# Kernel tuning notes

Measured on AMD Instinct MI355X. Metric: run time of the kernel, lower is better.

Reference implementation:

```python
import jax, jax.numpy as jnp
import numpy as np

# Decode-stage paged attention with ALiBi (HPU flat-PA style):
# batch2block scatter of queries, per-block QK + alibi bias, segment-wise
# stable softmax over each sequence's blocks, AV matmul, block2batch reduce.
BATCH = 32          # decode sequences
H = 32              # query heads
KVH = 8             # kv heads (GQA)
QPK = H // KVH      # queries per kv head
D = 128             # head size
BS = 128            # block size (tokens per KV-cache block)
BLOCKS_PER_SEQ = 16 # context 2048 tokens per sequence
U = BATCH * BLOCKS_PER_SEQ  # 512 used blocks
NB = 600            # total blocks in cache pool
SCALE = 1.0 / float(np.sqrt(D))
NEG = -1e30


def setup_inputs() -> dict:
    key = jax.random.key(0)
    k0, k1, k2 = jax.random.split(key, 3)
    query = jax.random.normal(k0, (BATCH, H, D), jnp.float32)
    key_cache = jax.random.normal(k1, (NB, BS, KVH, D), jnp.float32)
    value_cache = jax.random.normal(k2, (NB, BS, KVH, D), jnp.float32)
    # contiguous PA: used blocks are the first U blocks of the pool
    block_list = jnp.arange(U, dtype=jnp.int32)
    # each sequence owns BLOCKS_PER_SEQ consecutive blocks
    block_groups = (jnp.arange(U, dtype=jnp.int32) // BLOCKS_PER_SEQ).astype(jnp.int32)
    # all blocks fully used (context = BLOCKS_PER_SEQ*BS exactly)
    block_usage = jnp.full((U,), BS, dtype=jnp.int32)
    # alibi_blocks[u, p] = (global position) - (context_len - 1)  (<= 0)
    ctx = BLOCKS_PER_SEQ * BS
    pos = (jnp.arange(U) % BLOCKS_PER_SEQ)[:, None] * BS + jnp.arange(BS)[None, :]
    alibi_blocks = (pos - (ctx - 1)).astype(jnp.float32)
    # standard geometric alibi slopes: 2^(-8*(i+1)/H)
    alibi_slopes = 2.0 ** (-(jnp.arange(1, H + 1, dtype=jnp.float32)) * (8.0 / H))
    return dict(query=query, key_cache=key_cache, value_cache=value_cache,
                alibi_blocks=alibi_blocks, alibi_slopes=alibi_slopes,
                block_list=block_list, block_groups=block_groups,
                block_usage=block_usage)


def reference(query, key_cache, value_cache, alibi_blocks, alibi_slopes,
              block_list, block_groups, block_usage):
    # gather KV blocks from the paged cache
    K = key_cache[block_list]            # [U, BS, KVH, D]
    V = value_cache[block_list]          # [U, BS, KVH, D]
    # batch2block: replicate each sequence's query onto its blocks
    q = query[block_groups] * SCALE      # [U, H, D]
    qg = q.reshape(U, KVH, QPK, D)
    # QK^T per block (GQA: each kv head serves QPK query heads)
    scores = jnp.einsum('ugqd,ukgd->ugqk', qg, K).reshape(U, H, BS)
    # decode alibi bias: [U, H, BS] = alibi_blocks[:,None,:] * slopes[None,:,None]
    scores = scores + alibi_blocks[:, None, :] * alibi_slopes[None, :, None]
    # mask unused slots within each block
    valid = jnp.arange(BS, dtype=jnp.int32)[None, :] < block_usage[:, None]  # [U, BS]
    scores = jnp.where(valid[:, None, :], scores, NEG)
    # stable softmax across all blocks of each sequence (segment-wise)
    bmax = scores.max(-1)                                            # [U, H]
    gmax = jax.ops.segment_max(bmax, block_groups, num_segments=BATCH)
    e = jnp.exp(scores - gmax[block_groups][:, :, None])             # [U, H, BS]
    e = jnp.where(valid[:, None, :], e, 0.0)
    bsum = e.sum(-1)                                                 # [U, H]
    gsum = jax.ops.segment_sum(bsum, block_groups, num_segments=BATCH)  # [B, H]
    # AV per block, then block2batch reduce
    eg = e.reshape(U, KVH, QPK, BS)
    av = jnp.einsum('ugqk,ukgd->ugqd', eg, V).reshape(U, H, D)       # [U, H, D]
    out = jax.ops.segment_sum(av, block_groups, num_segments=BATCH)  # [B, H, D]
    out = out / gsum[:, :, None]
    return out.reshape(BATCH, H * D)
```

## Files before the change

kernel.cpp:

```cpp
#include <hip/hip_runtime.h>
#include <stdint.h>

#define BATCH 32
#define NH    32
#define KVH   8
#define QPK   4
#define DH    128
#define BS    128
#define NEG   (-1e30f)
#define SCALEF 0.08838834764831845f
#define MAXU  64
#define NSP   8
#define CHK   8
#define KVROW (KVH * DH)

#define GAS __attribute__((address_space(1)))
#define LAS __attribute__((address_space(3)))

#define LOAD_V(PB, VR) do {                                                     \
  const float* vb_ = value_cache + ((size_t)(PB) * BS + T0 + half) * KVROW      \
                   + g * DH + r32 * 4;                                          \
  _Pragma("unroll")                                                             \
  for (int tp = 0; tp < 4; ++tp)                                                \
    VR[tp] = *(const float4*)&vb_[(size_t)tp * 2 * KVROW];                      \
} while (0)

#define STAGE_K(PB, BUFI) do {                                                  \
  const float* kbase_ = key_cache + ((size_t)(PB) * BS + T0) * KVROW + g * DH;  \
  float* dst_ = &Kbuf[w][BUFI][0];                                              \
  _Pragma("unroll")                                                             \
  for (int seg = 0; seg < 4; ++seg) {                                           \
    const int t_  = 2 * seg + half;                                             \
    const int sg_ = r32 ^ t_;                                                   \
    __builtin_amdgcn_global_load_lds(                                           \
        (const GAS void*)(kbase_ + (size_t)t_ * KVROW + sg_ * 4),               \
        (LAS void*)(dst_ + seg * 256), 16, 0, 0);                               \
  }                                                                             \
} while (0)

#define COMPUTE(BUFI, ABV) do {                                                 \
  const float* kb_ = &Kbuf[w][BUFI][0];                                         \
  float a0_ = 0.f, a1_ = 0.f, a2_ = 0.f, a3_ = 0.f;                             \
  _Pragma("unroll")                                                             \
  for (int i = 0; i < 4; ++i) {                                                 \
    const int gi_  = oc * 4 + i;                                                \
    const int pos_ = gi_ ^ r8;                                                  \
    const float4 kv = *(const float4*)&kb_[r8 * DH + pos_ * 4];                 \
    const float4 q0 = *(const float4*)&q_lds[0 * DH + gi_ * 4];                 \
    const float4 q1 = *(const float4*)&q_lds[1 * DH + gi_ * 4];                 \
    const float4 q2 = *(const float4*)&q_lds[2 * DH + gi_ * 4];                 \
    const float4 q3 = *(const float4*)&q_lds[3 * DH + gi_ * 4];                 \
    a0_ += kv.x*q0.x + kv.y*q0.y + kv.z*q0.z + kv.w*q0.w;                       \
    a1_ += kv.x*q1.x + kv.y*q1.y + kv.z*q1.z + kv.w*q1.w;                       \
    a2_ += kv.x*q2.x + kv.y*q2.y + kv.z*q2.z + kv.w*q2.w;                       \
    a3_ += kv.x*q3.x + kv.y*q3.y + kv.z*q3.z + kv.w*q3.w;                       \
  }                                                                             \
  float accv_[QPK] = {a0_, a1_, a2_, a3_};                                      \
  const bool valid_ = (T0 + r8) < us_c;                                         \
  float pr_[QPK];                                                               \
  _Pragma("unroll")                                                             \
  for (int qh = 0; qh < QPK; ++qh) {                                            \
    float sc = accv_[qh];                                                       \
    sc += __shfl_xor(sc, 8);  sc += __shfl_xor(sc, 16); sc += __shfl_xor(sc, 32);\
    sc += (ABV) * slope[qh];                                                    \
    if (!valid_) sc = NEG;                                                      \
    float cm = fmaxf(sc, __shfl_xor(sc, 1));                                    \
    cm = fmaxf(cm, __shfl_xor(cm, 2)); cm = fmaxf(cm, __shfl_xor(cm, 4));       \
    const float mnew = fmaxf(m[qh], cm);                                        \
    const float rs = __expf(m[qh] - mnew);                                      \
    m[qh] = mnew;                                                               \
    pr_[qh] = valid_ ? __expf(sc - mnew) : 0.f;                                 \
    sacc[qh] = sacc[qh] * rs + ((lane < 8) ? pr_[qh] : 0.f);                    \
    O[qh][0] *= rs; O[qh][1] *= rs; O[qh][2] *= rs; O[qh][3] *= rs;             \
  }                                                                             \
  if (lane < 8)                                                                 \
    *(float4*)&p_lds[w][r8 * 4] = make_float4(pr_[0], pr_[1], pr_[2], pr_[3]);  \
} while (0)

#define AV(VR) do {                                                             \
  _Pragma("unroll")                                                             \
  for (int tp = 0; tp < 4; ++tp) {                                              \
    const float4 pv = *(const float4*)&p_lds[w][(2 * tp + half) * 4];           \
    const float4 vv = VR[tp];                                                   \
    O[0][0]+=pv.x*vv.x; O[0][1]+=pv.x*vv.y; O[0][2]+=pv.x*vv.z; O[0][3]+=pv.x*vv.w; \
    O[1][0]+=pv.y*vv.x; O[1][1]+=pv.y*vv.y; O[1][2]+=pv.y*vv.z; O[1][3]+=pv.y*vv.w; \
    O[2][0]+=pv.z*vv.x; O[2][1]+=pv.z*vv.y; O[2][2]+=pv.z*vv.z; O[2][3]+=pv.z*vv.w; \
    O[3][0]+=pv.w*vv.x; O[3][1]+=pv.w*vv.y; O[3][2]+=pv.w*vv.z; O[3][3]+=pv.w*vv.w; \
  }                                                                             \
} while (0)

#define BODY(VCUR, VNXT, BUFC, BUFN, CIDX) do {                                 \
  __builtin_amdgcn_sched_barrier(0);                                            \
  asm volatile("s_waitcnt vmcnt(0)" ::: "memory");                              \
  __builtin_amdgcn_sched_barrier(0);                                            \
  const bool hn_ = (CIDX) + 1 < nblk;                                           \
  int u_n = 0, pb_n = 0, us_n = 0; float ab_n = 0.f;                            \
  if (hn_) {                                                                    \
    u_n = ulist[(CIDX) + 1]; pb_n = pblds[(CIDX) + 1]; us_n = uslds[(CIDX) + 1];\
    LOAD_V(pb_n, VNXT);                                                         \
    ab_n = alibi_blocks[(size_t)u_n * BS + T0 + r8];                            \
    __builtin_amdgcn_sched_barrier(0);                                          \
    STAGE_K(pb_n, BUFN);                                                        \
    __builtin_amdgcn_sched_barrier(0);                                          \
  }                                                                             \
  COMPUTE(BUFC, ab_c);                                                          \
  AV(VCUR);                                                                     \
  u_c = u_n; pb_c = pb_n; us_c = us_n; ab_c = ab_n;                             \
} while (0)

__global__ __launch_bounds__(128, 4)
void pa_partial(const float* __restrict__ query,
                const float* __restrict__ key_cache,
                const float* __restrict__ value_cache,
                const float* __restrict__ alibi_blocks,
                const float* __restrict__ alibi_slopes,
                const int* __restrict__ block_list,
                const int* __restrict__ block_groups,
                const int* __restrict__ block_usage,
                float* __restrict__ Mp, float* __restrict__ Sp,
                float* __restrict__ Op, int U) {
  __shared__ __align__(16) float Kbuf[2][2][CHK * DH];
  __shared__ __align__(16) float q_lds[QPK * DH];
  __shared__ __align__(16) float p_lds[2][CHK * QPK];
  __shared__ int ulist[MAXU], pblds[MAXU], uslds[MAXU];
  __shared__ int ucount;

  const int tid  = threadIdx.x;
  const int w    = tid >> 6;
  const int lane = tid & 63;
  const int r32  = lane & 31;
  const int half = lane >> 5;
  const int r8   = lane & 7;
  const int oc   = lane >> 3;
  const int bid  = blockIdx.x;
  const int b    = bid >> 6;
  const int g    = (bid >> 3) & 7;
  const int s    = bid & 7;
  const int T0   = s * 16 + w * CHK;

  if (w == 0) {
    int cnt = 0;
    for (int base = 0; base < U; base += 64) {
      const int u = base + lane;
      const bool match = (u < U) && (block_groups[u] == b);
      const unsigned long long mk = __ballot(match);
      if (match) {
        const int pre = __popcll(mk & ((1ull << lane) - 1ull));
        if (cnt + pre < MAXU) ulist[cnt + pre] = u;
      }
      cnt += __popcll(mk);
    }
    if (cnt > MAXU) cnt = MAXU;
    if (lane == 0) ucount = cnt;
    for (int i = lane; i < cnt; i += 64) {
      const int u = ulist[i];
      pblds[i] = block_list[u];
      uslds[i] = block_usage[u];
    }
  }

  {
    const float* qsrc = query + ((size_t)b * NH + g * QPK) * DH;
    for (int e = tid; e < QPK * DH; e += 128) q_lds[e] = qsrc[e] * SCALEF;
  }

  float slope[QPK];
#pragma unroll
  for (int qh = 0; qh < QPK; ++qh) slope[qh] = alibi_slopes[g * QPK + qh];

  __syncthreads();

  const int nblk = ucount;

  float m[QPK], sacc[QPK], O[QPK][4];
#pragma unroll
  for (int qh = 0; qh < QPK; ++qh) {
    m[qh] = NEG; sacc[qh] = 0.f;
#pragma unroll
    for (int k = 0; k < 4; ++k) O[qh][k] = 0.f;
  }

  float4 vA[4], vB[4];
  int u_c = 0, pb_c = 0, us_c = 0;
  float ab_c = 0.f;

  if (nblk > 0) {
    u_c = ulist[0]; pb_c = pblds[0]; us_c = uslds[0];
    LOAD_V(pb_c, vA);
    ab_c = alibi_blocks[(size_t)u_c * BS + T0 + r8];
    STAGE_K(pb_c, 0);
  }

  for (int c = 0; c < nblk; c += 2) {
    BODY(vA, vB, 0, 1, c);
    if (c + 1 < nblk) BODY(vB, vA, 1, 0, c + 1);
  }

  float* cO  = &Kbuf[w][0][0];
  float* cMS = &Kbuf[w][1][0];
#pragma unroll
  for (int qh = 0; qh < QPK; ++qh) {
    float sv = sacc[qh];
#pragma unroll
    for (int off = 1; off < 64; off <<= 1) sv += __shfl_xor(sv, off);
#pragma unroll
    for (int k = 0; k < 4; ++k) O[qh][k] += __shfl_xor(O[qh][k], 32);
    if (half == 0) {
#pragma unroll
      for (int k = 0; k < 4; ++k) cO[qh * DH + r32 * 4 + k] = O[qh][k];
    }
    if (lane == 0) { cMS[qh] = m[qh]; cMS[4 + qh] = sv; }
  }
  __syncthreads();

  for (int e = tid; e < QPK * DH; e += 128) {
    const int qh = e >> 7, d = e & 127;
    const float M  = fmaxf(Kbuf[0][1][qh], Kbuf[1][1][qh]);
    const float f0 = __expf(Kbuf[0][1][qh] - M);
    const float f1 = __expf(Kbuf[1][1][qh] - M);
    const float S  = f0 * Kbuf[0][1][4 + qh] + f1 * Kbuf[1][1][4 + qh];
    const float Ov = f0 * Kbuf[0][0][qh * DH + d] + f1 * Kbuf[1][0][qh * DH + d];
    const int P = ((b * KVH + g) * QPK + qh) * NSP + s;
    Op[(size_t)P * DH + d] = Ov;
    if (d == 0) { Mp[P] = M; Sp[P] = S; }
  }
}

__global__ __launch_bounds__(256, 1)
void pa_combine(const float* __restrict__ Mp, const float* __restrict__ Sp,
                const float* __restrict__ Op, float* __restrict__ out) {
  const int e  = blockIdx.x * 256 + threadIdx.x;
  const int d  = e & 127;
  const int h  = (e >> 7) & 31;
  const int bb = e >> 12;
  const int gg = h >> 2, qh = h & 3;
  const int P  = ((bb * KVH + gg) * QPK + qh) * NSP;
  float M = NEG;
#pragma unroll
  for (int sp = 0; sp < NSP; ++sp) M = fmaxf(M, Mp[P + sp]);
  float S = 0.f, Ov = 0.f;
#pragma unroll
  for (int sp = 0; sp < NSP; ++sp) {
    const float f = __expf(Mp[P + sp] - M);
    S  += f * Sp[P + sp];
    Ov += f * Op[(size_t)(P + sp) * DH + d];
  }
  out[e] = Ov / S;
}

extern "C" void kernel_launch(void* const* d_in, const int* in_sizes, int n_in,
                              void* d_out, int out_size, void* d_ws, size_t ws_size,
                              hipStream_t stream) {
  (void)n_in; (void)out_size; (void)ws_size;
  const float* query        = (const float*)d_in[0];
  const float* key_cache    = (const float*)d_in[1];
  const float* value_cache  = (const float*)d_in[2];
  const float* alibi_blocks = (const float*)d_in[3];
  const float* alibi_slopes = (const float*)d_in[4];
  const int*   block_list   = (const int*)d_in[5];
  const int*   block_groups = (const int*)d_in[6];
  const int*   block_usage  = (const int*)d_in[7];
  float*       out          = (float*)d_out;
  const int U = in_sizes[5];

  const int NP = BATCH * KVH * QPK * NSP;
  float* Mp = (float*)d_ws;
  float* Sp = Mp + NP;
  float* Op = Sp + NP;

  pa_partial<<<dim3(BATCH * KVH * NSP), dim3(128), 0, stream>>>(
      query, key_cache, value_cache, alibi_blocks, alibi_slopes,
      block_list, block_groups, block_usage, Mp, Sp, Op, U);

  pa_combine<<<dim3(BATCH * NH * DH / 256), dim3(256), 0, stream>>>(Mp, Sp, Op, out);
}
```

Before: 119.4 us.

## Double per-wave token chunk, halve sequence splits, and reorder prefetch with partial waitcnt

Each wave now handles 16 tokens per block instead of 8, and the sequence is split into 4 workgroups instead of 8, giving half as many blocks with more work each. The body issues the next K stage into LDS first and waits only on older loads (vmcnt(9)). The next V register load and the alibi fetch are moved after the QK compute, so they overlap with the softmax and AV math. The query LDS layout is padded to avoid bank conflicts in the new indexing. Launch bounds drop to 2 waves per EU to fit the doubled V register buffers, which lowers occupancy and halves grid parallelism.

```diff
diff --git a/kernel.cpp b/kernel.cpp
--- a/kernel.cpp
+++ b/kernel.cpp
@@ -10,26 +10,19 @@
 #define NEG   (-1e30f)
 #define SCALEF 0.08838834764831845f
 #define MAXU  64
-#define NSP   8
-#define CHK   8
+#define NSP   4
+#define CHK   16
 #define KVROW (KVH * DH)
 
 #define GAS __attribute__((address_space(1)))
 #define LAS __attribute__((address_space(3)))
 
-#define LOAD_V(PB, VR) do {                                                     \
-  const float* vb_ = value_cache + ((size_t)(PB) * BS + T0 + half) * KVROW      \
-                   + g * DH + r32 * 4;                                          \
-  _Pragma("unroll")                                                             \
-  for (int tp = 0; tp < 4; ++tp)                                                \
-    VR[tp] = *(const float4*)&vb_[(size_t)tp * 2 * KVROW];                      \
-} while (0)
 
 #define STAGE_K(PB, BUFI) do {                                                  \
   const float* kbase_ = key_cache + ((size_t)(PB) * BS + T0) * KVROW + g * DH;  \
   float* dst_ = &Kbuf[w][BUFI][0];                                              \
   _Pragma("unroll")                                                             \
-  for (int seg = 0; seg < 4; ++seg) {                                           \
+  for (int seg = 0; seg < 8; ++seg) {                                           \
     const int t_  = 2 * seg + half;                                             \
     const int sg_ = r32 ^ t_;                                                   \
     __builtin_amdgcn_global_load_lds(                                           \
@@ -38,77 +31,90 @@
   }                                                                             \
 } while (0)
 
-#define COMPUTE(BUFI, ABV) do {                                                 \
-  const float* kb_ = &Kbuf[w][BUFI][0];                                         \
+#define LOAD_V(PB, VR) do {                                                     \
+  const float* vb_ = value_cache + ((size_t)(PB) * BS + T0 + half) * KVROW      \
+                   + g * DH + r32 * 4;                                          \
+  _Pragma("unroll")                                                             \
+  for (int tp = 0; tp < 8; ++tp)                                                \
+    VR[tp] = *(const float4*)&vb_[(size_t)tp * 2 * KVROW];                      \
+} while (0)
+
+#define BODY(CIDX, BUFC, BUFN, VCUR, VNXT) do {                                 \
+  __builtin_amdgcn_sched_barrier(0);                                            \
+  asm volatile("s_waitcnt vmcnt(9)" ::: "memory");                              \
+  __builtin_amdgcn_sched_barrier(0);                                            \
+  const bool hn_ = (CIDX) + 1 < nblk;                                           \
+  int u_n_ = 0, pb_n_ = 0, us_n_ = 0;                                           \
+  if (hn_) {                                                                    \
+    u_n_ = ulist[(CIDX) + 1]; pb_n_ = pblds[(CIDX) + 1];                        \
+    us_n_ = uslds[(CIDX) + 1];                                                  \
+    STAGE_K(pb_n_, BUFN);                                                       \
+  }                                                                             \
+  __builtin_amdgcn_sched_barrier(0);                                            \
+         \
   float a0_ = 0.f, a1_ = 0.f, a2_ = 0.f, a3_ = 0.f;                             \
+  {                                                                             \
+    const float* kb_ = &Kbuf[w][BUFC][0];                                       \
+    _Pragma("unroll")                                                           \
+    for (int i = 0; i < 8; ++i) {                                               \
+      const int pos_ = (dq * 8 + i) ^ r16;                                      \
+      const float4 kv = *(const float4*)&kb_[r16 * DH + pos_ * 4];              \
+      const float4 q0 = *(const float4*)&q_lds[((0 * 4 + dq) * 9 + i) * 4];     \
+      const float4 q1 = *(const float4*)&q_lds[((1 * 4 + dq) * 9 + i) * 4];     \
+      const float4 q2 = *(const float4*)&q_lds[((2 * 4 + dq) * 9 + i) * 4];     \
+      const float4 q3 = *(const float4*)&q_lds[((3 * 4 + dq) * 9 + i) * 4];     \
+      a0_ += kv.x*q0.x + kv.y*q0.y + kv.z*q0.z + kv.w*q0.w;                     \
+      a1_ += kv.x*q1.x + kv.y*q1.y + kv.z*q1.z + kv.w*q1.w;                     \
+      a2_ += kv.x*q2.x + kv.y*q2.y + kv.z*q2.z + kv.w*q2.w;                     \
+      a3_ += kv.x*q3.x + kv.y*q3.y + kv.z*q3.z + kv.w*q3.w;                     \
+    }                                                                           \
+  }                                                                             \
+          \
+  float ab_n_ = 0.f;                                                            \
+  if (hn_) {                                                                    \
+    LOAD_V(pb_n_, VNXT);                                                        \
+    ab_n_ = alibi_blocks[(size_t)u_n_ * BS + T0 + r16];                         \
+  }                                                                             \
+               \
+  {                                                                             \
+    float accv_[QPK] = {a0_, a1_, a2_, a3_};                                    \
+    const bool valid_ = (T0 + r16) < us_c;                                      \
+    float pr_[QPK];                                                             \
+    _Pragma("unroll")                                                           \
+    for (int qh = 0; qh < QPK; ++qh) {                                          \
+      float sc = accv_[qh] + __shfl_xor(accv_[qh], 16);                         \
+      sc += __shfl_xor(sc, 32);                                                 \
+      sc += ab_c * slope[qh];                                                   \
+      if (!valid_) sc = NEG;                                                    \
+      float cm = sc;                                                            \
+      _Pragma("unroll")                                                         \
+      for (int off = 1; off < 16; off <<= 1)                                    \
+        cm = fmaxf(cm, __shfl_xor(cm, off));                                    \
+      const float mnew = fmaxf(m[qh], cm);                                      \
+      const float rs   = __expf(m[qh] - mnew);                                  \
+      m[qh] = mnew;                                                             \
+      pr_[qh] = valid_ ? __expf(sc - mnew) : 0.f;                               \
+      sacc[qh] = sacc[qh] * rs + ((lane < 16) ? pr_[qh] : 0.f);                 \
+      O[qh][0] *= rs; O[qh][1] *= rs; O[qh][2] *= rs; O[qh][3] *= rs;           \
+    }                                                                           \
+    if (lane < 16)                                                              \
+      *(float4*)&p_lds[w][r16 * 4] =                                            \
+          make_float4(pr_[0], pr_[1], pr_[2], pr_[3]);                          \
+  }                                                                             \
+             \
   _Pragma("unroll")                                                             \
-  for (int i = 0; i < 4; ++i) {                                                 \
-    const int gi_  = oc * 4 + i;                                                \
-    const int pos_ = gi_ ^ r8;                                                  \
-    const float4 kv = *(const float4*)&kb_[r8 * DH + pos_ * 4];                 \
-    const float4 q0 = *(const float4*)&q_lds[0 * DH + gi_ * 4];                 \
-    const float4 q1 = *(const float4*)&q_lds[1 * DH + gi_ * 4];                 \
-    const float4 q2 = *(const float4*)&q_lds[2 * DH + gi_ * 4];                 \
-    const float4 q3 = *(const float4*)&q_lds[3 * DH + gi_ * 4];                 \
-    a0_ += kv.x*q0.x + kv.y*q0.y + kv.z*q0.z + kv.w*q0.w;                       \
-    a1_ += kv.x*q1.x + kv.y*q1.y + kv.z*q1.z + kv.w*q1.w;                       \
-    a2_ += kv.x*q2.x + kv.y*q2.y + kv.z*q2.z + kv.w*q2.w;                       \
-    a3_ += kv.x*q3.x + kv.y*q3.y + kv.z*q3.z + kv.w*q3.w;                       \
-  }                                                                             \
-  float accv_[QPK] = {a0_, a1_, a2_, a3_};                                      \
-  const bool valid_ = (T0 + r8) < us_c;                                         \
-  float pr_[QPK];                                                               \
-  _Pragma("unroll")                                                             \
-  for (int qh = 0; qh < QPK; ++qh) {                                            \
-    float sc = accv_[qh];                                                       \
-    sc += __shfl_xor(sc, 8);  sc += __shfl_xor(sc, 16); sc += __shfl_xor(sc, 32);\
-    sc += (ABV) * slope[qh];                                                    \
-    if (!valid_) sc = NEG;                                                      \
-    float cm = fmaxf(sc, __shfl_xor(sc, 1));                                    \
-    cm = fmaxf(cm, __shfl_xor(cm, 2)); cm = fmaxf(cm, __shfl_xor(cm, 4));       \
-    const float mnew = fmaxf(m[qh], cm);                                        \
-    const float rs = __expf(m[qh] - mnew);                                      \
-    m[qh] = mnew;                                                               \
-    pr_[qh] = valid_ ? __expf(sc - mnew) : 0.f;                                 \
-    sacc[qh] = sacc[qh] * rs + ((lane < 8) ? pr_[qh] : 0.f);                    \
-    O[qh][0] *= rs; O[qh][1] *= rs; O[qh][2] *= rs; O[qh][3] *= rs;             \
-  }                                                                             \
-  if (lane < 8)                                                                 \
-    *(float4*)&p_lds[w][r8 * 4] = make_float4(pr_[0], pr_[1], pr_[2], pr_[3]);  \
-} while (0)
-
-#define AV(VR) do {                                                             \
-  _Pragma("unroll")                                                             \
-  for (int tp = 0; tp < 4; ++tp) {                                              \
+  for (int tp = 0; tp < 8; ++tp) {                                              \
     const float4 pv = *(const float4*)&p_lds[w][(2 * tp + half) * 4];           \
-    const float4 vv = VR[tp];                                                   \
+    const float4 vv = VCUR[tp];                                                 \
     O[0][0]+=pv.x*vv.x; O[0][1]+=pv.x*vv.y; O[0][2]+=pv.x*vv.z; O[0][3]+=pv.x*vv.w; \
     O[1][0]+=pv.y*vv.x; O[1][1]+=pv.y*vv.y; O[1][2]+=pv.y*vv.z; O[1][3]+=pv.y*vv.w; \
     O[2][0]+=pv.z*vv.x; O[2][1]+=pv.z*vv.y; O[2][2]+=pv.z*vv.z; O[2][3]+=pv.z*vv.w; \
     O[3][0]+=pv.w*vv.x; O[3][1]+=pv.w*vv.y; O[3][2]+=pv.w*vv.z; O[3][3]+=pv.w*vv.w; \
   }                                                                             \
+  us_c = us_n_; ab_c = ab_n_;                                                   \
 } while (0)
 
-#define BODY(VCUR, VNXT, BUFC, BUFN, CIDX) do {                                 \
-  __builtin_amdgcn_sched_barrier(0);                                            \
-  asm volatile("s_waitcnt vmcnt(0)" ::: "memory");                              \
-  __builtin_amdgcn_sched_barrier(0);                                            \
-  const bool hn_ = (CIDX) + 1 < nblk;                                           \
-  int u_n = 0, pb_n = 0, us_n = 0; float ab_n = 0.f;                            \
-  if (hn_) {                                                                    \
-    u_n = ulist[(CIDX) + 1]; pb_n = pblds[(CIDX) + 1]; us_n = uslds[(CIDX) + 1];\
-    LOAD_V(pb_n, VNXT);                                                         \
-    ab_n = alibi_blocks[(size_t)u_n * BS + T0 + r8];                            \
-    __builtin_amdgcn_sched_barrier(0);                                          \
-    STAGE_K(pb_n, BUFN);                                                        \
-    __builtin_amdgcn_sched_barrier(0);                                          \
-  }                                                                             \
-  COMPUTE(BUFC, ab_c);                                                          \
-  AV(VCUR);                                                                     \
-  u_c = u_n; pb_c = pb_n; us_c = us_n; ab_c = ab_n;                             \
-} while (0)
-
-__global__ __launch_bounds__(128, 4)
+__global__ __launch_bounds__(128, 2)
 void pa_partial(const float* __restrict__ query,
                 const float* __restrict__ key_cache,
                 const float* __restrict__ value_cache,
@@ -120,7 +126,7 @@
                 float* __restrict__ Mp, float* __restrict__ Sp,
                 float* __restrict__ Op, int U) {
   __shared__ __align__(16) float Kbuf[2][2][CHK * DH];
-  __shared__ __align__(16) float q_lds[QPK * DH];
+  __shared__ __align__(16) float q_lds[QPK * 4 * 9 * 4];
   __shared__ __align__(16) float p_lds[2][CHK * QPK];
   __shared__ int ulist[MAXU], pblds[MAXU], uslds[MAXU];
   __shared__ int ucount;
@@ -130,13 +136,13 @@
   const int lane = tid & 63;
   const int r32  = lane & 31;
   const int half = lane >> 5;
-  const int r8   = lane & 7;
-  const int oc   = lane >> 3;
+  const int r16  = lane & 15;
+  const int dq   = lane >> 4;
   const int bid  = blockIdx.x;
-  const int b    = bid >> 6;
-  const int g    = (bid >> 3) & 7;
-  const int s    = bid & 7;
-  const int T0   = s * 16 + w * CHK;
+  const int b    = bid >> 5;
+  const int g    = (bid >> 2) & 7;
+  const int s    = bid & 3;
+  const int T0   = s * 32 + w * CHK;
 
   if (w == 0) {
     int cnt = 0;
@@ -161,7 +167,11 @@
 
   {
     const float* qsrc = query + ((size_t)b * NH + g * QPK) * DH;
-    for (int e = tid; e < QPK * DH; e += 128) q_lds[e] = qsrc[e] * SCALEF;
+    for (int e = tid; e < QPK * DH; e += 128) {
+      const int qh = e >> 7, idx = e & 127;
+      const int qq = idx >> 5, ii = (idx >> 2) & 7, kk = idx & 3;
+      q_lds[((qh * 4 + qq) * 9 + ii) * 4 + kk] = qsrc[e] * SCALEF;
+    }
   }
 
   float slope[QPK];
@@ -180,20 +190,22 @@
     for (int k = 0; k < 4; ++k) O[qh][k] = 0.f;
   }
 
-  float4 vA[4], vB[4];
-  int u_c = 0, pb_c = 0, us_c = 0;
+  float4 vA[8], vB[8];
+  int us_c = 0;
   float ab_c = 0.f;
 
   if (nblk > 0) {
-    u_c = ulist[0]; pb_c = pblds[0]; us_c = uslds[0];
-    LOAD_V(pb_c, vA);
-    ab_c = alibi_blocks[(size_t)u_c * BS + T0 + r8];
-    STAGE_K(pb_c, 0);
+    const int u0 = ulist[0], pb0 = pblds[0];
+    us_c = uslds[0];
+    STAGE_K(pb0, 0);
+    __builtin_amdgcn_sched_barrier(0);
+    LOAD_V(pb0, vA);
+    ab_c = alibi_blocks[(size_t)u0 * BS + T0 + r16];
   }
 
   for (int c = 0; c < nblk; c += 2) {
-    BODY(vA, vB, 0, 1, c);
-    if (c + 1 < nblk) BODY(vB, vA, 1, 0, c + 1);
+    BODY(c, 0, 1, vA, vB);
+    if (c + 1 < nblk) BODY(c + 1, 1, 0, vB, vA);
   }
 
   float* cO  = &Kbuf[w][0][0];
```

After: 248.9 us. +108.4%, slower.
